# Kernel optimization log

Hardware: AMD Instinct MI355X
Metric: run time of the kernel (lower is better)

## Reference

```python
import jax, jax.numpy as jnp
import numpy as np

N_NODES = 50000
N_EDGES = 800000
NODE_FEAT = 176
EDGE_FEAT = 4
HIDDEN = 64
LAYERS = 4
LN_EPS = 1e-5


def setup_inputs() -> dict:
    key = jax.random.key(0)
    ks = jax.random.split(key, 20)
    H, H2, Hh = HIDDEN, HIDDEN * 2, HIDDEN // 2
    inp = {
        "x": jax.random.normal(ks[0], (N_NODES, NODE_FEAT), jnp.float32),
        "edge_index": jax.random.randint(ks[1], (2, N_EDGES), 0, N_NODES, jnp.int64),
        "edge_attr": jax.random.normal(ks[2], (N_EDGES, EDGE_FEAT), jnp.float32),
        # input projection
        "in_w": jax.random.normal(ks[3], (NODE_FEAT, H), jnp.float32) * 0.05,
        "in_b": jnp.zeros((H,), jnp.float32),
        # per-layer GINEConv params (stacked over LAYERS)
        "edge_w": jax.random.normal(ks[4], (LAYERS, EDGE_FEAT, H), jnp.float32) * 0.1,
        "edge_b": jnp.zeros((LAYERS, H), jnp.float32),
        "mlp_w1": jax.random.normal(ks[5], (LAYERS, H, H2), jnp.float32) * 0.05,
        "mlp_b1": jnp.zeros((LAYERS, H2), jnp.float32),
        "mlp_w2": jax.random.normal(ks[6], (LAYERS, H2, H), jnp.float32) * 0.05,
        "mlp_b2": jnp.zeros((LAYERS, H), jnp.float32),
        "ln_g": jnp.ones((LAYERS, H), jnp.float32),
        "ln_b": jnp.zeros((LAYERS, H), jnp.float32),
        "reg_w1": jax.random.normal(ks[7], (H, Hh), jnp.float32) * 0.1,
        "reg_b1": jnp.zeros((Hh,), jnp.float32),
        "reg_w2": jax.random.normal(ks[8], (Hh, 1), jnp.float32) * 0.1,
        "reg_b2": jnp.zeros((1,), jnp.float32),
    }
    return inp


def _layernorm(z, g, b):
    mu = jnp.mean(z, axis=-1, keepdims=True)
    var = jnp.mean((z - mu) ** 2, axis=-1, keepdims=True)
    return g * (z - mu) * jax.lax.rsqrt(var + LN_EPS) + b


def reference(x, edge_index, edge_attr, in_w, in_b, edge_w, edge_b,
              mlp_w1, mlp_b1, mlp_w2, mlp_b2, ln_g, ln_b,
              reg_w1, reg_b1, reg_w2, reg_b2):
    src, dst = edge_index[0], edge_index[1]
    h = x @ in_w + in_b  # [N, H]
    for l in range(LAYERS):
        e = edge_attr @ edge_w[l] + edge_b[l]              # [E, H] edge projection
        msg = jax.nn.relu(h[src] + e)                      # gather + relu
        aggr = jax.ops.segment_sum(msg, dst, num_segments=h.shape[0])  # scatter-add
        z = h + aggr                                       # (1+eps)*x_i + aggr, eps=0
        z = jax.nn.relu(z @ mlp_w1[l] + mlp_b1[l]) @ mlp_w2[l] + mlp_b2[l]
        h = jax.nn.relu(_layernorm(z, ln_g[l], ln_b[l]))
    g = jnp.sum(h, axis=0)                                 # global_add_pool, single graph
    out = jax.nn.relu(g @ reg_w1 + reg_b1) @ reg_w2 + reg_b2
    return out.squeeze()
```

## Files before the change

### kernel.cpp

```cpp
#include <hip/hip_runtime.h>

#define N_NODES 50000
#define N_EDGES 800000
#define NODE_FEAT 176
#define HIDDEN 64
#define LN_EPS 1e-5f
#define SCAN_NB 49

typedef short bf16x8 __attribute__((ext_vector_type(8)));
typedef float f32x4 __attribute__((ext_vector_type(4)));

__device__ __forceinline__ unsigned short f2bf(float f) {
    unsigned int u = __float_as_uint(f);
    u += 0x7FFFu + ((u >> 16) & 1u);
    return (unsigned short)(u >> 16);
}
__device__ __forceinline__ int pack2(float lo, float hi) {
    return (int)(((unsigned)f2bf(hi) << 16) | (unsigned)f2bf(lo));
}
__device__ __forceinline__ float bf2f(unsigned short s) {
    return __uint_as_float(((unsigned int)s) << 16);
}
__device__ __forceinline__ float wave_sum64(float v) {
#pragma unroll
    for (int o = 32; o > 0; o >>= 1) v += __shfl_xor(v, o);
    return v;
}
__device__ __forceinline__ float sum16(float v) {
#pragma unroll
    for (int o = 8; o > 0; o >>= 1) v += __shfl_xor(v, o);
    return v;
}

__global__ __launch_bounds__(256) void k_wprep(const float* __restrict__ in_w,
                                               const float* __restrict__ w1,
                                               const float* __restrict__ w2,
                                               unsigned short* __restrict__ fin,
                                               unsigned short* __restrict__ f1,
                                               unsigned short* __restrict__ f2,
                                               int* __restrict__ cnt) {
    int t = blockIdx.x * 256 + threadIdx.x;
    if (t < N_NODES) cnt[t] = 0;
    if (t < 12288) {
        int e = t;
        int r = e & 7, lane = (e >> 3) & 63, j = (e >> 9) & 3, s = e >> 11;
        int k = s * 32 + ((lane >> 4) << 3) + r;
        int n = (j << 4) + (lane & 15);
        fin[e] = (k < NODE_FEAT) ? f2bf(in_w[k * 64 + n]) : (unsigned short)0;
    } else if (t < 12288 + 32768) {
        int e = t - 12288;
        int L = e >> 13, e2 = e & 8191;
        int r = e2 & 7, lane = (e2 >> 3) & 63, j = (e2 >> 9) & 7, s = (e2 >> 12) & 1;
        int k = s * 32 + ((lane >> 4) << 3) + r;
        int n = (j << 4) + (lane & 15);
        f1[e] = f2bf(w1[L * 8192 + k * 128 + n]);
    } else if (t < 12288 + 32768 + 32768) {
        int e = t - 45056;
        int L = e >> 13, e2 = e & 8191;
        int r = e2 & 7, lane = (e2 >> 3) & 63, j = (e2 >> 9) & 3, s = (e2 >> 11) & 3;
        int k = s * 32 + ((lane >> 4) << 3) + r;
        int n = (j << 4) + (lane & 15);
        f2[e] = f2bf(w2[L * 8192 + k * 64 + n]);
    }
}

__global__ __launch_bounds__(256) void k_inproj_mfma(const float* __restrict__ x,
                                                     const unsigned short* __restrict__ wfrag,
                                                     const float* __restrict__ in_b,
                                                     unsigned short* __restrict__ hb) {
    __shared__ unsigned short lw[12288];
    const int tid = threadIdx.x;
    {
        const bf16x8* src = (const bf16x8*)wfrag;
        bf16x8* dst = (bf16x8*)lw;
        for (int i = tid; i < 1536; i += 256) dst[i] = src[i];
    }
    __syncthreads();
    const int wv = tid >> 6, lane = tid & 63;
    const int lrow = lane & 15, lgrp = lane >> 4;
    float ib[4];
#pragma unroll
    for (int j = 0; j < 4; ++j) ib[j] = in_b[16 * j + lrow];
    const int nwaves = gridDim.x * 4;
    for (int tile = blockIdx.x * 4 + wv; tile < 3125; tile += nwaves) {
        const int m0 = tile * 16;
        f32x4 acc[4];
#pragma unroll
        for (int j = 0; j < 4; ++j) acc[j] = (f32x4){ib[j], ib[j], ib[j], ib[j]};
#pragma unroll
        for (int s = 0; s < 6; ++s) {
            const int kbase = s * 32 + lgrp * 8;
            bf16x8 a;
            if (kbase < NODE_FEAT) {
                const float* p = x + (size_t)(m0 + lrow) * NODE_FEAT + kbase;
                float4 fa = *(const float4*)p;
                float4 fb = *(const float4*)(p + 4);
                a[0] = (short)f2bf(fa.x); a[1] = (short)f2bf(fa.y);
                a[2] = (short)f2bf(fa.z); a[3] = (short)f2bf(fa.w);
                a[4] = (short)f2bf(fb.x); a[5] = (short)f2bf(fb.y);
                a[6] = (short)f2bf(fb.z); a[7] = (short)f2bf(fb.w);
            } else {
                a = (bf16x8){0, 0, 0, 0, 0, 0, 0, 0};
            }
#pragma unroll
            for (int j = 0; j < 4; ++j) {
                bf16x8 b = *(const bf16x8*)&lw[((s * 4 + j) * 64 + lane) * 8];
                acc[j] = __builtin_amdgcn_mfma_f32_16x16x32_bf16(a, b, acc[j], 0, 0, 0);
            }
        }
#pragma unroll
        for (int j = 0; j < 4; ++j) {
            const int col = 16 * j + lrow;
#pragma unroll
            for (int r = 0; r < 4; ++r) {
                const int node = m0 + lgrp * 4 + r;
                hb[(size_t)node * 64 + col] = f2bf(acc[j][r]);
            }
        }
    }
}

__global__ __launch_bounds__(256) void k_hist(const int* __restrict__ ei,
                                              int* __restrict__ cnt,
                                              int* __restrict__ erank) {
    int e = blockIdx.x * 256 + threadIdx.x;
    if (e < N_EDGES) erank[e] = atomicAdd(&cnt[ei[N_EDGES + e]], 1);
}

__global__ __launch_bounds__(256) void k_scan_part(const int* __restrict__ cnt,
                                                   int* __restrict__ blksum) {
    const int b = blockIdx.x, t = threadIdx.x;
    const int base = b * 1024 + t * 4;
    int s = 0;
#pragma unroll
    for (int i = 0; i < 4; ++i) {
        int idx = base + i;
        if (idx < N_NODES) s += cnt[idx];
    }
#pragma unroll
    for (int o = 32; o > 0; o >>= 1) s += __shfl_xor(s, o);
    __shared__ int wt[4];
    if ((t & 63) == 0) wt[t >> 6] = s;
    __syncthreads();
    if (t == 0) blksum[b] = wt[0] + wt[1] + wt[2] + wt[3];
}

__global__ __launch_bounds__(64) void k_scan_top(const int* __restrict__ blksum,
                                                 int* __restrict__ blkoff,
                                                 int* __restrict__ row_last) {
    const int t = threadIdx.x;
    int v = (t < SCAN_NB) ? blksum[t] : 0;
    int incl = v;
#pragma unroll
    for (int o = 1; o < 64; o <<= 1) {
        int u = __shfl_up(incl, o);
        if (t >= o) incl += u;
    }
    if (t < SCAN_NB) blkoff[t] = incl - v;
    if (t == 63) row_last[0] = incl;
}

__global__ __launch_bounds__(256) void k_scan_add(const int* __restrict__ cnt,
                                                  const int* __restrict__ blkoff,
                                                  int* __restrict__ row_ptr) {
    const int b = blockIdx.x, t = threadIdx.x;
    const int base = b * 1024 + t * 4;
    int c[4];
    int tsum = 0;
#pragma unroll
    for (int i = 0; i < 4; ++i) {
        int idx = base + i;
        c[i] = (idx < N_NODES) ? cnt[idx] : 0;
        tsum += c[i];
    }
    int incl = tsum;
#pragma unroll
    for (int o = 1; o < 64; o <<= 1) {
        int u = __shfl_up(incl, o);
        if ((t & 63) >= o) incl += u;
    }
    __shared__ int wt[4];
    const int wv = t >> 6;
    if ((t & 63) == 63) wt[wv] = incl;
    __syncthreads();
    int run = blkoff[b] + (incl - tsum);
    for (int w = 0; w < wv; ++w) run += wt[w];
#pragma unroll
    for (int i = 0; i < 4; ++i) {
        int idx = base + i;
        if (idx < N_NODES) row_ptr[idx] = run;
        run += c[i];
    }
}

__global__ __launch_bounds__(256) void k_scatter(const int* __restrict__ ei,
                                                 const float4* __restrict__ ea,
                                                 const int* __restrict__ row_ptr,
                                                 const int* __restrict__ erank,
                                                 int4* __restrict__ rec) {
    int e = blockIdx.x * 256 + threadIdx.x;
    if (e >= N_EDGES) return;
    int d = ei[N_EDGES + e];
    float4 a = ea[e];
    int4 r;
    r.x = pack2(a.x, a.y);
    r.y = pack2(a.z, a.w);
    r.z = ei[e];
    r.w = 0;
    rec[row_ptr[d] + erank[e]] = r;
}

__global__ __launch_bounds__(256) void k_aggr(const unsigned short* __restrict__ hb_in,
                                              unsigned short* __restrict__ zb,
                                              const int* __restrict__ row_ptr,
                                              const int4* __restrict__ rec,
                                              const float* __restrict__ ew,
                                              const float* __restrict__ eb) {
    const int wv = threadIdx.x >> 6, lane = threadIdx.x & 63;
    const int node = blockIdx.x * 4 + wv;
    const float ew0 = ew[0 * 64 + lane], ew1 = ew[1 * 64 + lane];
    const float ew2 = ew[2 * 64 + lane], ew3 = ew[3 * 64 + lane];
    const float ebl = eb[lane];
    const int beg = __builtin_amdgcn_readfirstlane(row_ptr[node]);
    const int end = __builtin_amdgcn_readfirstlane(row_ptr[node + 1]);
    float acc = bf2f(hb_in[(size_t)node * 64 + lane]);
    int i = beg;
    for (; i + 16 <= end; i += 16) {
        int d0[16], d1[16], sx[16];
#pragma unroll
        for (int t = 0; t < 16; ++t) {
            int4 r = rec[i + t];
            d0[t] = __builtin_amdgcn_readfirstlane(r.x);
            d1[t] = __builtin_amdgcn_readfirstlane(r.y);
            sx[t] = __builtin_amdgcn_readfirstlane(r.z);
        }
        float gg[16];
#pragma unroll
        for (int t = 0; t < 16; ++t)
            gg[t] = bf2f(hb_in[((size_t)sx[t] << 6) + lane]);
#pragma unroll
        for (int t = 0; t < 16; ++t) {
            float a0 = __uint_as_float((unsigned)d0[t] << 16);
            float a1 = __uint_as_float((unsigned)d0[t] & 0xffff0000u);
            float a2 = __uint_as_float((unsigned)d1[t] << 16);
            float a3 = __uint_as_float((unsigned)d1[t] & 0xffff0000u);
            float v = fmaf(a0, ew0, fmaf(a1, ew1, fmaf(a2, ew2, fmaf(a3, ew3, ebl))));
            acc += fmaxf(v + gg[t], 0.0f);
        }
    }
    if (i < end) {
        const int n = end - i;
        int d0[16], d1[16], sx[16];
#pragma unroll
        for (int t = 0; t < 16; ++t) {
            int idx = i + ((t < n) ? t : (n - 1));
            int4 r = rec[idx];
            d0[t] = __builtin_amdgcn_readfirstlane(r.x);
            d1[t] = __builtin_amdgcn_readfirstlane(r.y);
            sx[t] = __builtin_amdgcn_readfirstlane(r.z);
        }
        float gg[16];
#pragma unroll
        for (int t = 0; t < 16; ++t)
            gg[t] = bf2f(hb_in[((size_t)sx[t] << 6) + lane]);
#pragma unroll
        for (int t = 0; t < 16; ++t) {
            float m = (t < n) ? 1.0f : 0.0f;
            float a0 = __uint_as_float((unsigned)d0[t] << 16);
            float a1 = __uint_as_float((unsigned)d0[t] & 0xffff0000u);
            float a2 = __uint_as_float((unsigned)d1[t] << 16);
            float a3 = __uint_as_float((unsigned)d1[t] & 0xffff0000u);
            float v = fmaf(a0, ew0, fmaf(a1, ew1, fmaf(a2, ew2, fmaf(a3, ew3, ebl))));
            acc += m * fmaxf(v + gg[t], 0.0f);
        }
    }
    zb[(size_t)node * 64 + lane] = f2bf(acc);
}

__global__ __launch_bounds__(256) void k_mlp_mfma(const unsigned short* __restrict__ zb,
                                                  unsigned short* __restrict__ hb_out,
                                                  const unsigned short* __restrict__ f1,
                                                  const unsigned short* __restrict__ f2,
                                                  const float* __restrict__ b1,
                                                  const float* __restrict__ b2,
                                                  const float* __restrict__ lng,
                                                  const float* __restrict__ lnb) {
    __shared__ unsigned short w1f[8192];
    __shared__ unsigned short w2f[8192];
    __shared__ unsigned short z1s[4][2048];
    const int tid = threadIdx.x;
    {
        const bf16x8* s1 = (const bf16x8*)f1;
        const bf16x8* s2 = (const bf16x8*)f2;
        bf16x8* d1 = (bf16x8*)w1f;
        bf16x8* d2 = (bf16x8*)w2f;
        for (int i = tid; i < 1024; i += 256) { d1[i] = s1[i]; d2[i] = s2[i]; }
    }
    __syncthreads();
    const int wv = tid >> 6, lane = tid & 63;
    const int lrow = lane & 15, lgrp = lane >> 4;
    unsigned short* zs = z1s[wv];
    float bb1[8], bb2[4], g4[4], be4[4];
#pragma unroll
    for (int j = 0; j < 8; ++j) bb1[j] = b1[16 * j + lrow];
#pragma unroll
    for (int j = 0; j < 4; ++j) {
        bb2[j] = b2[16 * j + lrow];
        g4[j] = lng[16 * j + lrow];
        be4[j] = lnb[16 * j + lrow];
    }
    const int nwaves = gridDim.x * 4;
    for (int tile = blockIdx.x * 4 + wv; tile < 3125; tile += nwaves) {
        const int m0 = tile * 16;
        f32x4 acc1[8];
#pragma unroll
        for (int j = 0; j < 8; ++j) acc1[j] = (f32x4){bb1[j], bb1[j], bb1[j], bb1[j]};
#pragma unroll
        for (int s = 0; s < 2; ++s) {
            const int kbase = s * 32 + lgrp * 8;
            bf16x8 a = *(const bf16x8*)&zb[(size_t)(m0 + lrow) * 64 + kbase];
#pragma unroll
            for (int j = 0; j < 8; ++j) {
                bf16x8 b = *(const bf16x8*)&w1f[((s * 8 + j) * 64 + lane) * 8];
                acc1[j] = __builtin_amdgcn_mfma_f32_16x16x32_bf16(a, b, acc1[j], 0, 0, 0);
            }
        }
#pragma unroll
        for (int j = 0; j < 8; ++j) {
            const int col = 16 * j + lrow;
#pragma unroll
            for (int r = 0; r < 4; ++r) {
                const int row = lgrp * 4 + r;
                const int idx = (row * 128 + col) ^ ((row & 7) << 3);
                zs[idx] = f2bf(fmaxf(acc1[j][r], 0.0f));
            }
        }
        f32x4 acc2[4];
#pragma unroll
        for (int j = 0; j < 4; ++j) acc2[j] = (f32x4){bb2[j], bb2[j], bb2[j], bb2[j]};
#pragma unroll
        for (int s = 0; s < 4; ++s) {
            const int kbase = s * 32 + lgrp * 8;
            const int idx = (lrow * 128 + kbase) ^ ((lrow & 7) << 3);
            bf16x8 a = *(const bf16x8*)&zs[idx];
#pragma unroll
            for (int j = 0; j < 4; ++j) {
                bf16x8 b = *(const bf16x8*)&w2f[((s * 4 + j) * 64 + lane) * 8];
                acc2[j] = __builtin_amdgcn_mfma_f32_16x16x32_bf16(a, b, acc2[j], 0, 0, 0);
            }
        }
#pragma unroll
        for (int r = 0; r < 4; ++r) {
            float sum = acc2[0][r] + acc2[1][r] + acc2[2][r] + acc2[3][r];
            sum = sum16(sum);
            const float mu = sum * (1.0f / 64.0f);
            float sq = 0.0f;
#pragma unroll
            for (int j = 0; j < 4; ++j) {
                float d = acc2[j][r] - mu;
                sq = fmaf(d, d, sq);
            }
            sq = sum16(sq);
            const float rstd = rsqrtf(sq * (1.0f / 64.0f) + LN_EPS);
            const int node = m0 + lgrp * 4 + r;
#pragma unroll
            for (int j = 0; j < 4; ++j) {
                const int col = 16 * j + lrow;
                float d = acc2[j][r] - mu;
                float hn = fmaxf(fmaf(g4[j] * d, rstd, be4[j]), 0.0f);
                hb_out[(size_t)node * 64 + col] = f2bf(hn);
            }
        }
    }
}

__global__ __launch_bounds__(256) void k_pool(const unsigned short* __restrict__ hb,
                                              float* __restrict__ gpart) {
    __shared__ float red[256];
    const int tid = threadIdx.x;
    const int lane = tid & 63;
    float part = 0.0f;
    for (int i = blockIdx.x * 4 + (tid >> 6); i < N_NODES; i += gridDim.x * 4)
        part += bf2f(hb[(size_t)i * 64 + lane]);
    red[tid] = part;
    __syncthreads();
    if (tid < 64) {
        gpart[blockIdx.x * 64 + tid] = red[tid] + red[tid + 64] + red[tid + 128] + red[tid + 192];
    }
}

__global__ __launch_bounds__(64) void k_reg(const float* __restrict__ gpart,
                                            const float* __restrict__ w1,
                                            const float* __restrict__ b1,
                                            const float* __restrict__ w2,
                                            const float* __restrict__ b2,
                                            float* __restrict__ out) {
    const int j = threadIdx.x;
    float gj = 0.0f;
    for (int b = 0; b < 256; ++b) gj += gpart[b * 64 + j];
    __shared__ float gs[64];
    gs[j] = gj;
    __syncthreads();
    const int jm = j & 31;
    float acc = b1[jm];
#pragma unroll 8
    for (int k = 0; k < 64; ++k) {
        float gk = gs[k];
        acc = fmaf(gk, w1[k * 32 + jm], acc);
    }
    float contrib = (j < 32) ? fmaxf(acc, 0.0f) * w2[jm] : 0.0f;
    float s = wave_sum64(contrib);
    if (j == 0) out[0] = s + b2[0];
}

extern "C" void kernel_launch(void* const* d_in, const int* in_sizes, int n_in,
                              void* d_out, int out_size, void* d_ws, size_t ws_size,
                              hipStream_t stream) {
    const float* x      = (const float*)d_in[0];
    const int*   ei     = (const int*)d_in[1];
    const float* ea     = (const float*)d_in[2];
    const float* in_w   = (const float*)d_in[3];
    const float* in_b   = (const float*)d_in[4];
    const float* edge_w = (const float*)d_in[5];
    const float* edge_b = (const float*)d_in[6];
    const float* mlp_w1 = (const float*)d_in[7];
    const float* mlp_b1 = (const float*)d_in[8];
    const float* mlp_w2 = (const float*)d_in[9];
    const float* mlp_b2 = (const float*)d_in[10];
    const float* ln_g   = (const float*)d_in[11];
    const float* ln_b   = (const float*)d_in[12];
    const float* reg_w1 = (const float*)d_in[13];
    const float* reg_b1 = (const float*)d_in[14];
    const float* reg_w2 = (const float*)d_in[15];
    const float* reg_b2 = (const float*)d_in[16];

    char* ws = (char*)d_ws;
    unsigned short* hb0     = (unsigned short*)ws; ws += (size_t)N_NODES * 64 * 2;
    unsigned short* hb1     = (unsigned short*)ws; ws += (size_t)N_NODES * 64 * 2;
    unsigned short* zb      = (unsigned short*)ws; ws += (size_t)N_NODES * 64 * 2;
    int4*           rec     = (int4*)ws;           ws += (size_t)N_EDGES * 16;
    unsigned short* fin     = (unsigned short*)ws; ws += 12288 * 2;
    unsigned short* f1      = (unsigned short*)ws; ws += 32768 * 2;
    unsigned short* f2      = (unsigned short*)ws; ws += 32768 * 2;
    int*            erank   = (int*)ws;            ws += (size_t)N_EDGES * 4;
    int*            row_ptr = (int*)ws;            ws += (size_t)(N_NODES + 1) * 4;
    int*            cnt     = (int*)ws;            ws += (size_t)N_NODES * 4;
    int*            blksum  = (int*)ws;            ws += SCAN_NB * 4;
    int*            blkoff  = (int*)ws;            ws += SCAN_NB * 4;
    float*          gpart   = (float*)ws;          ws += 256 * 64 * 4;
    float*          outf    = (float*)d_out;

    const int eb_blocks = (N_EDGES + 255) / 256;

    k_wprep<<<304, 256, 0, stream>>>(in_w, mlp_w1, mlp_w2, fin, f1, f2, cnt);

    k_hist<<<eb_blocks, 256, 0, stream>>>(ei, cnt, erank);
    k_scan_part<<<SCAN_NB, 256, 0, stream>>>(cnt, blksum);
    k_scan_top<<<1, 64, 0, stream>>>(blksum, blkoff, row_ptr + N_NODES);
    k_scan_add<<<SCAN_NB, 256, 0, stream>>>(cnt, blkoff, row_ptr);
    k_scatter<<<eb_blocks, 256, 0, stream>>>(ei, (const float4*)ea, row_ptr, erank, rec);

    k_inproj_mfma<<<512, 256, 0, stream>>>(x, fin, in_b, hb0);

    unsigned short* hbA = hb0;
    unsigned short* hbB = hb1;
    for (int l = 0; l < 4; ++l) {
        k_aggr<<<N_NODES / 4, 256, 0, stream>>>(hbA, zb, row_ptr, rec,
                                                edge_w + l * 4 * 64,
                                                edge_b + l * 64);
        k_mlp_mfma<<<768, 256, 0, stream>>>(zb, hbB,
                                            f1 + l * 8192, f2 + l * 8192,
                                            mlp_b1 + l * 128, mlp_b2 + l * 64,
                                            ln_g + l * 64, ln_b + l * 64);
        unsigned short* tb = hbA; hbA = hbB; hbB = tb;
    }

    k_pool<<<256, 256, 0, stream>>>(hbA, gpart);
    k_reg<<<1, 64, 0, stream>>>(gpart, reg_w1, reg_b1, reg_w2, reg_b2, outf);
}
```

Before: 297.3 us.

## Gather neighbor features from an FP8 copy and add nontemporal hints

The input projection and the MLP kernels now write a second copy of the node features in FP8 next to the bf16 copy. The aggregation kernel gathers neighbor rows from this FP8 copy, which halves the bytes fetched per random neighbor access. The self term still reads the bf16 copy. The gather unroll drops from 16 to 8, and nontemporal hints are added to the record loads and the feature stores. The cost is extra FP8 store traffic, reduced precision in the messages (a possible accuracy risk), and less memory-level parallelism per wave.

```diff
diff --git a/kernel.cpp b/kernel.cpp
--- a/kernel.cpp
+++ b/kernel.cpp
@@ -9,6 +9,7 @@
 
 typedef short bf16x8 __attribute__((ext_vector_type(8)));
 typedef float f32x4 __attribute__((ext_vector_type(4)));
+typedef long long ll2 __attribute__((ext_vector_type(2)));
 
 __device__ __forceinline__ unsigned short f2bf(float f) {
     unsigned int u = __float_as_uint(f);
@@ -21,6 +22,45 @@
 __device__ __forceinline__ float bf2f(unsigned short s) {
     return __uint_as_float(((unsigned int)s) << 16);
 }
+
+#if __has_builtin(__builtin_amdgcn_cvt_pk_fp8_f32) && __has_builtin(__builtin_amdgcn_cvt_f32_fp8)
+#define HW_FP8 1
+#endif
+
+__device__ __forceinline__ unsigned char f2fp8(float f) {
+#ifdef HW_FP8
+    return (unsigned char)(__builtin_amdgcn_cvt_pk_fp8_f32(f, f, 0, false) & 0xff);
+#else
+    unsigned u = __float_as_uint(f);
+    unsigned s = (u >> 24) & 0x80u;
+    float a = fabsf(f);
+    if (a >= 448.f) return (unsigned char)(s | 0x7E);
+    if (a < 0.0078125f) {
+        int m = (int)fmaf(a, 512.0f, 0.5f);
+        return (unsigned char)(s | (m > 7 ? 7 : m));
+    }
+    unsigned au = u & 0x7fffffffu;
+    au += 0x7ffffu + ((au >> 20) & 1u);
+    int e8 = (int)(au >> 23) - 120;
+    if (e8 <= 0) {
+        int m = (int)fmaf(__uint_as_float(au), 512.0f, 0.5f);
+        return (unsigned char)(s | (m > 7 ? 7 : m));
+    }
+    if (e8 > 15) return (unsigned char)(s | 0x7E);
+    return (unsigned char)(s | (e8 << 3) | ((au >> 20) & 7));
+#endif
+}
+__device__ __forceinline__ float fp82f(int b) {
+#ifdef HW_FP8
+    return __builtin_amdgcn_cvt_f32_fp8(b & 0xff, 0);
+#else
+    int s = (b >> 7) & 1, e = (b >> 3) & 15, m = b & 7;
+    float v = e ? __uint_as_float(((unsigned)(e + 120) << 23) | ((unsigned)m << 20))
+                : (float)m * 0.001953125f;
+    return s ? -v : v;
+#endif
+}
+
 __device__ __forceinline__ float wave_sum64(float v) {
 #pragma unroll
     for (int o = 32; o > 0; o >>= 1) v += __shfl_xor(v, o);
@@ -67,7 +107,8 @@
 __global__ __launch_bounds__(256) void k_inproj_mfma(const float* __restrict__ x,
                                                      const unsigned short* __restrict__ wfrag,
                                                      const float* __restrict__ in_b,
-                                                     unsigned short* __restrict__ hb) {
+                                                     unsigned short* __restrict__ hb,
+                                                     unsigned char* __restrict__ hf8) {
     __shared__ unsigned short lw[12288];
     const int tid = threadIdx.x;
     {
@@ -114,7 +155,9 @@
 #pragma unroll
             for (int r = 0; r < 4; ++r) {
                 const int node = m0 + lgrp * 4 + r;
-                hb[(size_t)node * 64 + col] = f2bf(acc[j][r]);
+                float v = acc[j][r];
+                __builtin_nontemporal_store(f2bf(v), &hb[(size_t)node * 64 + col]);
+                hf8[(size_t)node * 64 + col] = f2fp8(v);
             }
         }
     }
@@ -211,6 +254,7 @@
 }
 
 __global__ __launch_bounds__(256) void k_aggr(const unsigned short* __restrict__ hb_in,
+                                              const unsigned char* __restrict__ hf8_in,
                                               unsigned short* __restrict__ zb,
                                               const int* __restrict__ row_ptr,
                                               const int4* __restrict__ rec,
@@ -223,23 +267,23 @@
     const float ebl = eb[lane];
     const int beg = __builtin_amdgcn_readfirstlane(row_ptr[node]);
     const int end = __builtin_amdgcn_readfirstlane(row_ptr[node + 1]);
-    float acc = bf2f(hb_in[(size_t)node * 64 + lane]);
+    float acc = bf2f(__builtin_nontemporal_load(&hb_in[(size_t)node * 64 + lane]));
     int i = beg;
-    for (; i + 16 <= end; i += 16) {
-        int d0[16], d1[16], sx[16];
-#pragma unroll
-        for (int t = 0; t < 16; ++t) {
-            int4 r = rec[i + t];
-            d0[t] = __builtin_amdgcn_readfirstlane(r.x);
-            d1[t] = __builtin_amdgcn_readfirstlane(r.y);
-            sx[t] = __builtin_amdgcn_readfirstlane(r.z);
-        }
-        float gg[16];
-#pragma unroll
-        for (int t = 0; t < 16; ++t)
-            gg[t] = bf2f(hb_in[((size_t)sx[t] << 6) + lane]);
-#pragma unroll
-        for (int t = 0; t < 16; ++t) {
+    for (; i + 8 <= end; i += 8) {
+        int d0[8], d1[8], sx[8];
+#pragma unroll
+        for (int t = 0; t < 8; ++t) {
+            ll2 r = __builtin_nontemporal_load((const ll2*)(rec + i + t));
+            d0[t] = __builtin_amdgcn_readfirstlane((int)(r[0] & 0xffffffffLL));
+            d1[t] = __builtin_amdgcn_readfirstlane((int)(r[0] >> 32));
+            sx[t] = __builtin_amdgcn_readfirstlane((int)(r[1] & 0xffffffffLL));
+        }
+        float gg[8];
+#pragma unroll
+        for (int t = 0; t < 8; ++t)
+            gg[t] = fp82f(hf8_in[((size_t)sx[t] << 6) + lane]);
+#pragma unroll
+        for (int t = 0; t < 8; ++t) {
             float a0 = __uint_as_float((unsigned)d0[t] << 16);
             float a1 = __uint_as_float((unsigned)d0[t] & 0xffff0000u);
             float a2 = __uint_as_float((unsigned)d1[t] << 16);
@@ -250,21 +294,21 @@
     }
     if (i < end) {
         const int n = end - i;
-        int d0[16], d1[16], sx[16];
-#pragma unroll
-        for (int t = 0; t < 16; ++t) {
+        int d0[8], d1[8], sx[8];
+#pragma unroll
+        for (int t = 0; t < 8; ++t) {
             int idx = i + ((t < n) ? t : (n - 1));
-            int4 r = rec[idx];
-            d0[t] = __builtin_amdgcn_readfirstlane(r.x);
-            d1[t] = __builtin_amdgcn_readfirstlane(r.y);
-            sx[t] = __builtin_amdgcn_readfirstlane(r.z);
-        }
-        float gg[16];
-#pragma unroll
-        for (int t = 0; t < 16; ++t)
-            gg[t] = bf2f(hb_in[((size_t)sx[t] << 6) + lane]);
-#pragma unroll
-        for (int t = 0; t < 16; ++t) {
+            ll2 r = __builtin_nontemporal_load((const ll2*)(rec + idx));
+            d0[t] = __builtin_amdgcn_readfirstlane((int)(r[0] & 0xffffffffLL));
+            d1[t] = __builtin_amdgcn_readfirstlane((int)(r[0] >> 32));
+            sx[t] = __builtin_amdgcn_readfirstlane((int)(r[1] & 0xffffffffLL));
+        }
+        float gg[8];
+#pragma unroll
+        for (int t = 0; t < 8; ++t)
+            gg[t] = fp82f(hf8_in[((size_t)sx[t] << 6) + lane]);
+#pragma unroll
+        for (int t = 0; t < 8; ++t) {
             float m = (t < n) ? 1.0f : 0.0f;
             float a0 = __uint_as_float((unsigned)d0[t] << 16);
             float a1 = __uint_as_float((unsigned)d0[t] & 0xffff0000u);
@@ -274,11 +318,12 @@
             acc += m * fmaxf(v + gg[t], 0.0f);
         }
     }
-    zb[(size_t)node * 64 + lane] = f2bf(acc);
+    __builtin_nontemporal_store(f2bf(acc), &zb[(size_t)node * 64 + lane]);
 }
 
 __global__ __launch_bounds__(256) void k_mlp_mfma(const unsigned short* __restrict__ zb,
                                                   unsigned short* __restrict__ hb_out,
+                                                  unsigned char* __restrict__ hf8_out,
                                                   const unsigned short* __restrict__ f1,
                                                   const unsigned short* __restrict__ f2,
                                                   const float* __restrict__ b1,
@@ -368,7 +413,8 @@
                 const int col = 16 * j + lrow;
                 float d = acc2[j][r] - mu;
                 float hn = fmaxf(fmaf(g4[j] * d, rstd, be4[j]), 0.0f);
-                hb_out[(size_t)node * 64 + col] = f2bf(hn);
+                __builtin_nontemporal_store(f2bf(hn), &hb_out[(size_t)node * 64 + col]);
+                hf8_out[(size_t)node * 64 + col] = f2fp8(hn);
             }
         }
     }
@@ -438,6 +484,8 @@
     unsigned short* hb0     = (unsigned short*)ws; ws += (size_t)N_NODES * 64 * 2;
     unsigned short* hb1     = (unsigned short*)ws; ws += (size_t)N_NODES * 64 * 2;
     unsigned short* zb      = (unsigned short*)ws; ws += (size_t)N_NODES * 64 * 2;
+    unsigned char*  hf8_0   = (unsigned char*)ws;  ws += (size_t)N_NODES * 64;
+    unsigned char*  hf8_1   = (unsigned char*)ws;  ws += (size_t)N_NODES * 64;
     int4*           rec     = (int4*)ws;           ws += (size_t)N_EDGES * 16;
     unsigned short* fin     = (unsigned short*)ws; ws += 12288 * 2;
     unsigned short* f1      = (unsigned short*)ws; ws += 32768 * 2;
@@ -460,19 +508,22 @@
     k_scan_add<<<SCAN_NB, 256, 0, stream>>>(cnt, blkoff, row_ptr);
     k_scatter<<<eb_blocks, 256, 0, stream>>>(ei, (const float4*)ea, row_ptr, erank, rec);
 
-    k_inproj_mfma<<<512, 256, 0, stream>>>(x, fin, in_b, hb0);
+    k_inproj_mfma<<<512, 256, 0, stream>>>(x, fin, in_b, hb0, hf8_0);
 
     unsigned short* hbA = hb0;
     unsigned short* hbB = hb1;
+    unsigned char*  hfA = hf8_0;
+    unsigned char*  hfB = hf8_1;
     for (int l = 0; l < 4; ++l) {
-        k_aggr<<<N_NODES / 4, 256, 0, stream>>>(hbA, zb, row_ptr, rec,
+        k_aggr<<<N_NODES / 4, 256, 0, stream>>>(hbA, hfA, zb, row_ptr, rec,
                                                 edge_w + l * 4 * 64,
                                                 edge_b + l * 64);
-        k_mlp_mfma<<<768, 256, 0, stream>>>(zb, hbB,
+        k_mlp_mfma<<<768, 256, 0, stream>>>(zb, hbB, hfB,
                                             f1 + l * 8192, f2 + l * 8192,
                                             mlp_b1 + l * 128, mlp_b2 + l * 64,
                                             ln_g + l * 64, ln_b + l * 64);
         unsigned short* tb = hbA; hbA = hbB; hbB = tb;
+        unsigned char*  tf = hfA; hfA = hfB; hfB = tf;
     }
 
     k_pool<<<256, 256, 0, stream>>>(hbA, gpart);
```

Result: faster. 276.0 us (-7.2%).
